# Optimization experiments

Measured on AMD Instinct MI355X. Metric: run time of the kernel, lower is better.

Reference implementation:

```python
import jax, jax.numpy as jnp
import numpy as np

N_EMBED = 1024
N_HEAD = 16
HEAD_SIZE = N_EMBED // N_HEAD
LN_EPS = 1e-5


def setup_inputs() -> dict:
    key = jax.random.key(0)
    ks = jax.random.split(key, 12)
    B, T, C = 8, 1024, N_EMBED
    s = 0.02
    return {
        "x": jax.random.normal(ks[0], (B, T, C), dtype=jnp.float32),
        "Wq": jax.random.normal(ks[1], (C, C), dtype=jnp.float32) * s,
        "Wk": jax.random.normal(ks[2], (C, C), dtype=jnp.float32) * s,
        "Wv": jax.random.normal(ks[3], (C, C), dtype=jnp.float32) * s,
        "Wp": jax.random.normal(ks[4], (C, C), dtype=jnp.float32) * s,
        "bp": jnp.zeros((C,), dtype=jnp.float32),
        "ln1_g": jnp.ones((C,), dtype=jnp.float32),
        "ln1_b": jnp.zeros((C,), dtype=jnp.float32),
        "ln2_g": jnp.ones((C,), dtype=jnp.float32),
        "ln2_b": jnp.zeros((C,), dtype=jnp.float32),
        "W1": jax.random.normal(ks[5], (C, 4 * C), dtype=jnp.float32) * s,
        "b1": jnp.zeros((4 * C,), dtype=jnp.float32),
        "W2": jax.random.normal(ks[6], (4 * C, C), dtype=jnp.float32) * s,
        "b2": jnp.zeros((C,), dtype=jnp.float32),
    }


def _layernorm(x, g, b):
    mu = jnp.mean(x, axis=-1, keepdims=True)
    var = jnp.mean(jnp.square(x - mu), axis=-1, keepdims=True)
    return (x - mu) * jax.lax.rsqrt(var + LN_EPS) * g + b


def _block(x, Wq, Wk, Wv, Wp, bp, ln1_g, ln1_b, ln2_g, ln2_b, W1, b1, W2, b2):
    B, T, C = x.shape
    H, D = N_HEAD, HEAD_SIZE
    xn = _layernorm(x, ln1_g, ln1_b)
    # fused QKV for all heads (heads concatenated along feature dim, same as torch cat)
    q = (xn @ Wq).reshape(B, T, H, D)
    k = (xn @ Wk).reshape(B, T, H, D)
    v = (xn @ Wv).reshape(B, T, H, D)
    scores = jnp.einsum("bthd,bshd->bhts", q, k) / jnp.sqrt(jnp.float32(D))
    causal = jnp.tril(jnp.ones((T, T), dtype=bool))
    scores = jnp.where(causal, scores, jnp.float32(-jnp.inf))
    wei = jax.nn.softmax(scores, axis=-1)  # dropout = identity (eval)
    attn = jnp.einsum("bhts,bshd->bthd", wei, v).reshape(B, T, C)
    sa_out = attn @ Wp + bp  # dropout = identity (eval)
    x = x + sa_out
    xn2 = _layernorm(x, ln2_g, ln2_b)
    ff = jax.nn.relu(xn2 @ W1 + b1) @ W2 + b2  # dropout = identity (eval)
    return x + ff


def reference(x, Wq, Wk, Wv, Wp, bp, ln1_g, ln1_b, ln2_g, ln2_b, W1, b1, W2, b2):
    return _block(x, Wq, Wk, Wv, Wp, bp, ln1_g, ln1_b, ln2_g, ln2_b, W1, b1, W2, b2)
```

## Files before the change

kernel.cpp:

```cpp
#include <hip/hip_runtime.h>
#include <cstdint>
#include <cstddef>

using u16 = unsigned short;
typedef __attribute__((ext_vector_type(8))) short bh8;
typedef __attribute__((ext_vector_type(4))) float f4;

__device__ __forceinline__ u16 f2bf(float f) {
    union { float f; uint32_t u; } c; c.f = f;
    uint32_t u = c.u;
    u += 0x7FFFu + ((u >> 16) & 1u);
    return (u16)(u >> 16);
}

__device__ __forceinline__ void gload16(const void* g, void* l) {
    __builtin_amdgcn_global_load_lds(
        (__attribute__((address_space(1))) void*)g,
        (__attribute__((address_space(3))) void*)l,
        16, 0, 0);
}

__device__ __forceinline__ f4 mfma16(bh8 a, bh8 b, f4 c) {
    return __builtin_amdgcn_mfma_f32_16x16x32_bf16(a, b, c, 0, 0, 0);
}

__global__ __launch_bounds__(256) void wconv_kernel(
    const float* __restrict__ W, u16* __restrict__ Wt, int K, int N)
{
    __shared__ float t[32][33];
    const int tx = threadIdx.x & 31, ty = threadIdx.x >> 5;
    const int n0 = blockIdx.x * 32, k0 = blockIdx.y * 32;
#pragma unroll
    for (int j = 0; j < 4; ++j)
        t[ty + 8 * j][tx] = W[(size_t)(k0 + ty + 8 * j) * N + n0 + tx];
    __syncthreads();
#pragma unroll
    for (int j = 0; j < 4; ++j)
        Wt[(size_t)(n0 + ty + 8 * j) * K + k0 + tx] = f2bf(t[tx][ty + 8 * j]);
}

__global__ __launch_bounds__(256) void ln_kernel(
    const float* __restrict__ x, const float* __restrict__ g,
    const float* __restrict__ b, u16* __restrict__ out)
{
    const int row = blockIdx.x;
    const int tid = threadIdx.x;
    const float4 v = ((const float4*)(x + (size_t)row * 1024))[tid];
    float s  = v.x + v.y + v.z + v.w;
    float sq = v.x * v.x + v.y * v.y + v.z * v.z + v.w * v.w;
#pragma unroll
    for (int m = 1; m < 64; m <<= 1) {
        s  += __shfl_xor(s, m);
        sq += __shfl_xor(sq, m);
    }
    __shared__ float red[8];
    const int w = tid >> 6;
    if ((tid & 63) == 0) { red[w * 2] = s; red[w * 2 + 1] = sq; }
    __syncthreads();
    s  = red[0] + red[2] + red[4] + red[6];
    sq = red[1] + red[3] + red[5] + red[7];
    const float mu   = s * (1.0f / 1024.0f);
    const float var  = sq * (1.0f / 1024.0f) - mu * mu;
    const float rstd = rsqrtf(var + 1e-5f);
    const float4 gv = ((const float4*)g)[tid];
    const float4 bv = ((const float4*)b)[tid];
    ushort4 o;
    o.x = f2bf((v.x - mu) * rstd * gv.x + bv.x);
    o.y = f2bf((v.y - mu) * rstd * gv.y + bv.y);
    o.z = f2bf((v.z - mu) * rstd * gv.z + bv.z);
    o.w = f2bf((v.w - mu) * rstd * gv.w + bv.w);
    ((ushort4*)(out + (size_t)row * 1024))[tid] = o;
}

__global__ __launch_bounds__(256) void vtrans_kernel(
    const u16* __restrict__ vb, u16* __restrict__ vtb)
{
    __shared__ u16 t[64][66];
    const int bh = blockIdx.y;
    const int t0 = blockIdx.x * 64;
    const int b = bh >> 4, h = bh & 15;
    const u16* src = vb + (size_t)b * 1024 * 1024 + h * 64;
    const int rs = threadIdx.x >> 3, cs = threadIdx.x & 7;
#pragma unroll
    for (int it = 0; it < 2; ++it) {
        const int r = it * 32 + rs;
        *(uint4*)&t[r][cs * 8] = *(const uint4*)(src + (size_t)(t0 + r) * 1024 + cs * 8);
    }
    __syncthreads();
    u16* dst = vtb + (size_t)bh * 65536 + t0;
#pragma unroll
    for (int it = 0; it < 2; ++it) {
        const int d = it * 32 + rs;
        u16 tmp[8];
#pragma unroll
        for (int j = 0; j < 8; ++j) tmp[j] = t[cs * 8 + j][d];
        *(uint4*)(dst + (size_t)d * 1024 + cs * 8) = *(const uint4*)tmp;
    }
}

template <int EPI>
__global__ __launch_bounds__(256, 2) void gemm_kernel(
    const u16* __restrict__ A, const u16* __restrict__ Bt,
    int M, int N, int K,
    const float* __restrict__ bias, const float* __restrict__ resid,
    float* __restrict__ outf, u16* __restrict__ outb)
{
    __shared__ u16 Al[128 * 64];
    __shared__ u16 Bl[128 * 64];
    const int tid  = threadIdx.x;
    const int lane = tid & 63;
    const int w    = tid >> 6;
    const int wr   = w >> 1, wc = w & 1;
    const int mt   = blockIdx.y, nt = blockIdx.x;
    const int lrow = lane & 15;
    const int lkb  = (lane >> 4) * 8;
    const int rs   = tid >> 3;
    const int cs   = tid & 7;

    f4 acc[4][4] = {};

    for (int k0 = 0; k0 < K; k0 += 64) {
#pragma unroll
        for (int it = 0; it < 4; ++it) {
            const int r = it * 32 + rs;
            gload16(A + (size_t)(mt * 128 + r) * K + k0 + cs * 8,
                    (char*)Al + (it * 256 + w * 64) * 16);
        }
#pragma unroll
        for (int it = 0; it < 4; ++it) {
            const int r = it * 32 + rs;
            gload16(Bt + (size_t)(nt * 128 + r) * K + k0 + cs * 8,
                    (char*)Bl + (it * 256 + w * 64) * 16);
        }
        __syncthreads();
#pragma unroll
        for (int ks = 0; ks < 2; ++ks) {
            bh8 af[4], bv[4];
#pragma unroll
            for (int fm = 0; fm < 4; ++fm)
                af[fm] = *(const bh8*)&Al[(wr * 64 + fm * 16 + lrow) * 64 + ks * 32 + lkb];
#pragma unroll
            for (int fn = 0; fn < 4; ++fn)
                bv[fn] = *(const bh8*)&Bl[(wc * 64 + fn * 16 + lrow) * 64 + ks * 32 + lkb];
#pragma unroll
            for (int fm = 0; fm < 4; ++fm)
#pragma unroll
                for (int fn = 0; fn < 4; ++fn)
                    acc[fm][fn] = mfma16(af[fm], bv[fn], acc[fm][fn]);
        }
        __syncthreads();
    }

    const int r0 = mt * 128 + wr * 64 + (lane >> 4) * 4;
    const int c0 = nt * 128 + wc * 64 + lrow;
#pragma unroll
    for (int fn = 0; fn < 4; ++fn) {
        const int col = c0 + fn * 16;
        const float bvl = (EPI == 1 || EPI == 2) ? bias[col] : 0.0f;
#pragma unroll
        for (int fm = 0; fm < 4; ++fm) {
#pragma unroll
            for (int i = 0; i < 4; ++i) {
                const int rr = r0 + fm * 16 + i;
                const float v = acc[fm][fn][i];
                if (EPI == 0) {
                    outb[(size_t)rr * N + col] = f2bf(v);
                } else if (EPI == 1) {
                    const size_t idx = (size_t)rr * N + col;
                    outf[idx] = resid[idx] + v + bvl;
                } else if (EPI == 2) {
                    outb[(size_t)rr * N + col] = f2bf(fmaxf(v + bvl, 0.0f));
                } else {
                    outb[(size_t)(col >> 10) * 8388608 + (size_t)rr * 1024 + (col & 1023)]
                        = f2bf(v);
                }
            }
        }
    }
}

__global__ __launch_bounds__(256, 3) void attn_kernel(
    const u16* __restrict__ Q, const u16* __restrict__ K,
    const u16* __restrict__ Vt, u16* __restrict__ O)
{
    __shared__ u16 Kl[2][64 * 64];
    __shared__ u16 Vl[2][64 * 64];
    __shared__ u16 Pl[4][16 * 72];

    const int tid  = threadIdx.x;
    const int lane = tid & 63;
    const int w    = tid >> 6;
    const int bh   = blockIdx.y;
    const size_t base  = (size_t)(bh >> 4) * (1024 * 1024) + (bh & 15) * 64;
    const size_t vbase = (size_t)bh * 65536;
    const int lrow = lane & 15;
    const int lg   = lane >> 4;
    const int lkb  = lg * 8;
    const int rs   = tid >> 3, cs = tid & 7;

    const u16* Kp = K + base;
    const u16* Vp = Vt + vbase;

#pragma unroll 1
    for (int p = 0; p < 2; ++p) {
        const int qt = p ? (15 - blockIdx.x) : blockIdx.x;
        const int q0 = qt * 64;

        const bh8 aq0 = *(const bh8*)(Q + base + (size_t)(q0 + w * 16 + lrow) * 1024 + lkb);
        const bh8 aq1 = *(const bh8*)(Q + base + (size_t)(q0 + w * 16 + lrow) * 1024 + 32 + lkb);

        f4 o[4] = {};
        float mi[4], li[4];
#pragma unroll
        for (int i = 0; i < 4; ++i) { mi[i] = -__builtin_inff(); li[i] = 0.0f; }

#pragma unroll
        for (int it = 0; it < 2; ++it) {
            const int r = it * 32 + rs;
            gload16(Kp + (size_t)r * 1024 + ((cs ^ (r & 7)) * 8),
                    (char*)Kl[0] + it * 4096 + tid * 16);
            gload16(Vp + (size_t)r * 1024 + ((cs ^ (r & 7)) * 8),
                    (char*)Vl[0] + it * 4096 + tid * 16);
        }
        __syncthreads();

        for (int t = 0; t <= qt; ++t) {
            const int cur = t & 1;
            if (t < qt) {
                const int s1 = (t + 1) * 64;
#pragma unroll
                for (int it = 0; it < 2; ++it) {
                    const int r = it * 32 + rs;
                    gload16(Kp + (size_t)(s1 + r) * 1024 + ((cs ^ (r & 7)) * 8),
                            (char*)Kl[cur ^ 1] + it * 4096 + tid * 16);
                    gload16(Vp + (size_t)r * 1024 + s1 + ((cs ^ (r & 7)) * 8),
                            (char*)Vl[cur ^ 1] + it * 4096 + tid * 16);
                }
            }

            f4 sc[4] = {};
#pragma unroll
            for (int ks = 0; ks < 2; ++ks) {
                const bh8 a = ks ? aq1 : aq0;
#pragma unroll
                for (int fn = 0; fn < 4; ++fn) {
                    const int R = fn * 16 + lrow;
                    const bh8 bk = *(const bh8*)&Kl[cur][R * 64 + ((((ks << 2) + lg) ^ (R & 7)) * 8)];
                    sc[fn] = mfma16(a, bk, sc[fn]);
                }
            }
            const bool diag = (t == qt);
#pragma unroll
            for (int fn = 0; fn < 4; ++fn)
#pragma unroll
                for (int i = 0; i < 4; ++i) {
                    float v = sc[fn][i] * 0.125f;
                    if (diag) {
                        const int r = lg * 4 + i;
                        const int c = fn * 16 + lrow;
                        if (c > w * 16 + r) v = -__builtin_inff();
                    }
                    sc[fn][i] = v;
                }
#pragma unroll
            for (int i = 0; i < 4; ++i) {
                float pm = fmaxf(fmaxf(sc[0][i], sc[1][i]), fmaxf(sc[2][i], sc[3][i]));
#pragma unroll
                for (int m = 1; m < 16; m <<= 1) pm = fmaxf(pm, __shfl_xor(pm, m));
                const float mn   = fmaxf(mi[i], pm);
                const float corr = __expf(mi[i] - mn);
                float rsum = 0.0f;
#pragma unroll
                for (int fn = 0; fn < 4; ++fn) {
                    const float pv = __expf(sc[fn][i] - mn);
                    sc[fn][i] = pv;
                    rsum += pv;
                }
#pragma unroll
                for (int m = 1; m < 16; m <<= 1) rsum += __shfl_xor(rsum, m);
                li[i] = li[i] * corr + rsum;
                mi[i] = mn;
#pragma unroll
                for (int fn = 0; fn < 4; ++fn) o[fn][i] *= corr;
            }
#pragma unroll
            for (int fn = 0; fn < 4; ++fn)
#pragma unroll
                for (int i = 0; i < 4; ++i)
                    Pl[w][(lg * 4 + i) * 72 + fn * 16 + lrow] = f2bf(sc[fn][i]);
#pragma unroll
            for (int ss = 0; ss < 2; ++ss) {
                const bh8 ap = *(const bh8*)&Pl[w][lrow * 72 + ss * 32 + lkb];
#pragma unroll
                for (int fn = 0; fn < 4; ++fn) {
                    const int R = fn * 16 + lrow;
                    const bh8 bv = *(const bh8*)&Vl[cur][R * 64 + ((((ss << 2) + lg) ^ (R & 7)) * 8)];
                    o[fn] = mfma16(ap, bv, o[fn]);
                }
            }
            __syncthreads();
        }

#pragma unroll
        for (int fn = 0; fn < 4; ++fn)
#pragma unroll
            for (int i = 0; i < 4; ++i) {
                const int r = q0 + w * 16 + lg * 4 + i;
                const int c = fn * 16 + lrow;
                O[base + (size_t)r * 1024 + c] = f2bf(o[fn][i] / li[i]);
            }
    }
}

extern "C" void kernel_launch(void* const* d_in, const int* in_sizes, int n_in,
                              void* d_out, int out_size, void* d_ws, size_t ws_size,
                              hipStream_t stream) {
    const float* x    = (const float*)d_in[0];
    const float* Wq   = (const float*)d_in[1];
    const float* Wk   = (const float*)d_in[2];
    const float* Wv   = (const float*)d_in[3];
    const float* Wp   = (const float*)d_in[4];
    const float* bp   = (const float*)d_in[5];
    const float* ln1g = (const float*)d_in[6];
    const float* ln1b = (const float*)d_in[7];
    const float* ln2g = (const float*)d_in[8];
    const float* ln2b = (const float*)d_in[9];
    const float* W1   = (const float*)d_in[10];
    const float* b1   = (const float*)d_in[11];
    const float* W2   = (const float*)d_in[12];
    const float* b2   = (const float*)d_in[13];
    float* out = (float*)d_out;

    u16* ws   = (u16*)d_ws;
    u16* wqkt = ws;
    u16* wpt  = wqkt + (3u << 20);
    u16* w1t  = wpt  + (1u << 20);
    u16* w2t  = w1t  + (4u << 20);
    u16* qb   = w2t  + (4u << 20);
    u16* kb   = qb   + (8u << 20);
    u16* vb   = kb   + (8u << 20);
    u16* xnb  = vb   + (8u << 20);
    u16* vtb  = xnb;
    u16* aob  = vb;
    u16* xn2b = qb;
    u16* h1b  = kb;

    dim3 blk(256);
    wconv_kernel<<<dim3(32, 32),  blk, 0, stream>>>(Wq, wqkt,              1024, 1024);
    wconv_kernel<<<dim3(32, 32),  blk, 0, stream>>>(Wk, wqkt + (1u << 20), 1024, 1024);
    wconv_kernel<<<dim3(32, 32),  blk, 0, stream>>>(Wv, wqkt + (2u << 20), 1024, 1024);
    wconv_kernel<<<dim3(32, 32),  blk, 0, stream>>>(Wp, wpt, 1024, 1024);
    wconv_kernel<<<dim3(128, 32), blk, 0, stream>>>(W1, w1t, 1024, 4096);
    wconv_kernel<<<dim3(32, 128), blk, 0, stream>>>(W2, w2t, 4096, 1024);

    ln_kernel<<<8192, blk, 0, stream>>>(x, ln1g, ln1b, xnb);

    gemm_kernel<3><<<dim3(24, 64), blk, 0, stream>>>(xnb, wqkt, 8192, 3072, 1024,
                                                     nullptr, nullptr, nullptr, qb);

    vtrans_kernel<<<dim3(16, 128), blk, 0, stream>>>(vb, vtb);

    attn_kernel<<<dim3(8, 128), blk, 0, stream>>>(qb, kb, vtb, aob);

    gemm_kernel<1><<<dim3(8, 64), blk, 0, stream>>>(aob, wpt, 8192, 1024, 1024,
                                                    bp, x, out, nullptr);

    ln_kernel<<<8192, blk, 0, stream>>>(out, ln2g, ln2b, xn2b);

    gemm_kernel<2><<<dim3(32, 64), blk, 0, stream>>>(xn2b, w1t, 8192, 4096, 1024,
                                                     b1, nullptr, nullptr, h1b);
    gemm_kernel<1><<<dim3(8, 64), blk, 0, stream>>>(h1b, w2t, 8192, 1024, 4096,
                                                    b2, out, out, nullptr);
}
```

Measured before the change: 398.9 us.

## Replace GEMM with 8-wave 256-row tiles, triple-buffered LDS pipeline and XOR swizzle

Replaces the 128x128 single-buffered GEMM with a 512-thread kernel using 256xBN tiles, a three-slot LDS ring that prefetches two K-steps ahead, and interleaved A/B staging between the two MFMA halves. It adds an XOR swizzle on LDS layout to avoid bank conflicts, workgroup index swizzling for L2 locality, and s_setprio around the MFMA bursts. The aim is to hide global load latency and raise data reuse per tile. In exchange it needs more registers per wave and has fewer workgroups for the N=1024 GEMMs, and it relies on fragile hand-set vmcnt waits.

```diff
diff --git a/kernel.cpp b/kernel.cpp
--- a/kernel.cpp
+++ b/kernel.cpp
@@ -98,74 +98,125 @@
     }
 }
 
-template <int EPI>
-__global__ __launch_bounds__(256, 2) void gemm_kernel(
+template <int NF, int EPI>
+__global__ __launch_bounds__(512) void gemm8_kernel(
     const u16* __restrict__ A, const u16* __restrict__ Bt,
     int M, int N, int K,
     const float* __restrict__ bias, const float* __restrict__ resid,
     float* __restrict__ outf, u16* __restrict__ outb)
 {
-    __shared__ u16 Al[128 * 64];
-    __shared__ u16 Bl[128 * 64];
+    constexpr int BN = NF * 64;
+    __shared__ u16 Al[3][256 * 32];
+    __shared__ u16 Bl[3][BN * 32];
+
     const int tid  = threadIdx.x;
     const int lane = tid & 63;
     const int w    = tid >> 6;
-    const int wr   = w >> 1, wc = w & 1;
-    const int mt   = blockIdx.y, nt = blockIdx.x;
+    const int wr   = w >> 2;
+    const int wc   = w & 3;
     const int lrow = lane & 15;
-    const int lkb  = (lane >> 4) * 8;
-    const int rs   = tid >> 3;
-    const int cs   = tid & 7;
-
-    f4 acc[4][4] = {};
-
-    for (int k0 = 0; k0 < K; k0 += 64) {
-#pragma unroll
-        for (int it = 0; it < 4; ++it) {
-            const int r = it * 32 + rs;
-            gload16(A + (size_t)(mt * 128 + r) * K + k0 + cs * 8,
-                    (char*)Al + (it * 256 + w * 64) * 16);
-        }
-#pragma unroll
-        for (int it = 0; it < 4; ++it) {
-            const int r = it * 32 + rs;
-            gload16(Bt + (size_t)(nt * 128 + r) * K + k0 + cs * 8,
-                    (char*)Bl + (it * 256 + w * 64) * 16);
-        }
-        __syncthreads();
-#pragma unroll
-        for (int ks = 0; ks < 2; ++ks) {
-            bh8 af[4], bv[4];
-#pragma unroll
-            for (int fm = 0; fm < 4; ++fm)
-                af[fm] = *(const bh8*)&Al[(wr * 64 + fm * 16 + lrow) * 64 + ks * 32 + lkb];
-#pragma unroll
-            for (int fn = 0; fn < 4; ++fn)
-                bv[fn] = *(const bh8*)&Bl[(wc * 64 + fn * 16 + lrow) * 64 + ks * 32 + lkb];
-#pragma unroll
-            for (int fm = 0; fm < 4; ++fm)
-#pragma unroll
-                for (int fn = 0; fn < 4; ++fn)
-                    acc[fm][fn] = mfma16(af[fm], bv[fn], acc[fm][fn]);
-        }
-        __syncthreads();
-    }
-
-    const int r0 = mt * 128 + wr * 64 + (lane >> 4) * 4;
-    const int c0 = nt * 128 + wc * 64 + lrow;
-#pragma unroll
-    for (int fn = 0; fn < 4; ++fn) {
+    const int lg   = lane >> 4;
+
+    const int gx  = gridDim.x;
+    const int nwg = gx * gridDim.y;
+    const int lin = blockIdx.y * gx + blockIdx.x;
+    const int swz = (lin & 7) * (nwg >> 3) + (lin >> 3);
+    const int nt  = swz % gx, mt = swz / gx;
+
+    const int NT = K >> 5;
+
+    auto stageA = [&](int slot, int kt) {
+#pragma unroll
+        for (int it = 0; it < 2; ++it) {
+            const int r = it * 128 + (tid >> 2);
+            gload16(A + (size_t)(mt * 256 + r) * K + kt * 32 + (((tid & 3) ^ (r & 3)) << 3),
+                    (char*)Al[slot] + it * 8192 + tid * 16);
+        }
+    };
+    auto stageB = [&](int slot, int kt) {
+#pragma unroll
+        for (int it = 0; it < NF / 2; ++it) {
+            const int r = it * 128 + (tid >> 2);
+            gload16(Bt + (size_t)(nt * BN + r) * K + kt * 32 + (((tid & 3) ^ (r & 3)) << 3),
+                    (char*)Bl[slot] + it * 8192 + tid * 16);
+        }
+    };
+
+    f4 acc[8][NF] = {};
+    bh8 af[8];
+    bh8 bf[NF];
+
+    auto readFrags = [&](int slot) {
+#pragma unroll
+        for (int fm = 0; fm < 8; ++fm) {
+            const int R = wr * 128 + fm * 16 + lrow;
+            af[fm] = *(const bh8*)&Al[slot][R * 32 + ((lg ^ (R & 3)) << 3)];
+        }
+#pragma unroll
+        for (int fn = 0; fn < NF; ++fn) {
+            const int R = wc * (NF * 16) + fn * 16 + lrow;
+            bf[fn] = *(const bh8*)&Bl[slot][R * 32 + ((lg ^ (R & 3)) << 3)];
+        }
+    };
+    auto mfmaHalf = [&](int mh) {
+#pragma unroll
+        for (int fm = 0; fm < 4; ++fm)
+#pragma unroll
+            for (int fn = 0; fn < NF; ++fn)
+                acc[mh * 4 + fm][fn] = mfma16(af[mh * 4 + fm], bf[fn], acc[mh * 4 + fm][fn]);
+    };
+
+    stageA(0, 0); stageB(0, 0);
+    stageA(1, 1); stageB(1, 1);
+    if (NF == 4) asm volatile("s_waitcnt vmcnt(4)" ::: "memory");
+    else         asm volatile("s_waitcnt vmcnt(3)" ::: "memory");
+    __builtin_amdgcn_s_barrier();
+    __builtin_amdgcn_sched_barrier(0);
+
+    int rs3 = 0, ws3 = 2;
+    for (int t = 0; t < NT; ++t) {
+        const bool pf = (t + 2 < NT);
+        readFrags(rs3);
+        if (pf) stageA(ws3, t + 2);
+        __builtin_amdgcn_s_barrier();
+        asm volatile("s_waitcnt lgkmcnt(0)" ::: "memory");
+        __builtin_amdgcn_sched_barrier(0);
+        __builtin_amdgcn_s_setprio(1);
+        mfmaHalf(0);
+        __builtin_amdgcn_s_setprio(0);
+        __builtin_amdgcn_s_barrier();
+        __builtin_amdgcn_sched_barrier(0);
+        if (pf) stageB(ws3, t + 2);
+        __builtin_amdgcn_s_barrier();
+        __builtin_amdgcn_sched_barrier(0);
+        __builtin_amdgcn_s_setprio(1);
+        mfmaHalf(1);
+        __builtin_amdgcn_s_setprio(0);
+        if (pf) {
+            if (NF == 4) asm volatile("s_waitcnt vmcnt(4)" ::: "memory");
+            else         asm volatile("s_waitcnt vmcnt(3)" ::: "memory");
+        } else {
+            asm volatile("s_waitcnt vmcnt(0)" ::: "memory");
+        }
+        __builtin_amdgcn_s_barrier();
+        __builtin_amdgcn_sched_barrier(0);
+        if (++rs3 == 3) rs3 = 0;
+        if (++ws3 == 3) ws3 = 0;
+    }
+
+    const int r0 = mt * 256 + wr * 128 + lg * 4;
+    const int c0 = nt * BN + wc * (NF * 16) + lrow;
+#pragma unroll
+    for (int fn = 0; fn < NF; ++fn) {
         const int col = c0 + fn * 16;
         const float bvl = (EPI == 1 || EPI == 2) ? bias[col] : 0.0f;
 #pragma unroll
-        for (int fm = 0; fm < 4; ++fm) {
+        for (int fm = 0; fm < 8; ++fm) {
 #pragma unroll
             for (int i = 0; i < 4; ++i) {
                 const int rr = r0 + fm * 16 + i;
                 const float v = acc[fm][fn][i];
-                if (EPI == 0) {
-                    outb[(size_t)rr * N + col] = f2bf(v);
-                } else if (EPI == 1) {
+                if (EPI == 1) {
                     const size_t idx = (size_t)rr * N + col;
                     outf[idx] = resid[idx] + v + bvl;
                 } else if (EPI == 2) {
@@ -355,20 +406,20 @@
 
     ln_kernel<<<8192, blk, 0, stream>>>(x, ln1g, ln1b, xnb);
 
-    gemm_kernel<3><<<dim3(24, 64), blk, 0, stream>>>(xnb, wqkt, 8192, 3072, 1024,
-                                                     nullptr, nullptr, nullptr, qb);
+    gemm8_kernel<4, 3><<<dim3(12, 32), 512, 0, stream>>>(xnb, wqkt, 8192, 3072, 1024,
+                                                         nullptr, nullptr, nullptr, qb);
 
     vtrans_kernel<<<dim3(16, 128), blk, 0, stream>>>(vb, vtb);
 
     attn_kernel<<<dim3(8, 128), blk, 0, stream>>>(qb, kb, vtb, aob);
 
-    gemm_kernel<1><<<dim3(8, 64), blk, 0, stream>>>(aob, wpt, 8192, 1024, 1024,
-                                                    bp, x, out, nullptr);
+    gemm8_kernel<2, 1><<<dim3(8, 32), 512, 0, stream>>>(aob, wpt, 8192, 1024, 1024,
+                                                        bp, x, out, nullptr);
 
     ln_kernel<<<8192, blk, 0, stream>>>(out, ln2g, ln2b, xn2b);
 
-    gemm_kernel<2><<<dim3(32, 64), blk, 0, stream>>>(xn2b, w1t, 8192, 4096, 1024,
-                                                     b1, nullptr, nullptr, h1b);
-    gemm_kernel<1><<<dim3(8, 64), blk, 0, stream>>>(h1b, w2t, 8192, 1024, 4096,
-                                                    b2, out, out, nullptr);
-}
+    gemm8_kernel<4, 2><<<dim3(16, 32), 512, 0, stream>>>(xn2b, w1t, 8192, 4096, 1024,
+                                                         b1, nullptr, nullptr, h1b);
+    gemm8_kernel<2, 1><<<dim3(8, 32), 512, 0, stream>>>(h1b, w2t, 8192, 1024, 4096,
+                                                        b2, out, out, nullptr);
+}
```

New measurement: 426.8 us. +7.0%, slower.
